# Kernel optimization log

Hardware: AMD Instinct MI355X
Metric: run time of the kernel (lower is better)

The kernel has to match this reference:

```python
import jax, jax.numpy as jnp
import numpy as np

NEG = -1000.0  # fill value for unmatched (type_mask != ti) entries

B, N, R = 4, 48, 16
T = 2 * R + 1          # 33 transition channels
Nc, L = 80, 3          # chains, chain length
Nt, Ni = 16, 5         # triples, chains per triple (uniform c_sections)


def setup_inputs() -> dict:
    key = jax.random.key(0)
    k1, k2, k3, k4, k5 = jax.random.split(key, 5)
    transitions = jax.random.normal(k1, (B, N, N, T), dtype=jnp.float32)
    type_mask = jax.random.randint(k2, (B, N, N, R), 0, 2, dtype=jnp.int32)
    rules = jax.random.randint(k3, (Nc, L), 0, T, dtype=jnp.int32)
    # stacked per-triple weights [Nt, Ni] (orig: ParameterList of [Ni,1]) and biases [Nt]
    weights = jax.random.normal(k4, (Nt, Ni), dtype=jnp.float32) / np.sqrt(Ni)
    biases = jax.random.uniform(k5, (Nt,), dtype=jnp.float32, minval=-1.0, maxval=1.0)
    return {"transitions": transitions, "type_mask": type_mask, "rules": rules,
            "weights": weights, "biases": biases}


def path_scores(transitions, rules):
    """Tropical (max-plus) chain DP.
    transitions: [B,N,N,T], rules: [Nc,L] -> scores [B,N,N,Nc]
    scores[b,x,y,c] = max over intermediate nodes of sum of hop scores.
    """
    Lc = rules.shape[1]
    hops = [transitions[..., rules[:, l]] for l in range(Lc)]  # each [B,N,N,Nc]
    # max-plus "matmul": s[b,x,y,c] = max_k hops0[b,x,k,c] + hops1[b,k,y,c]
    s = jnp.max(hops[0][:, :, :, None, :] + hops[1][:, None, :, :, :], axis=2)
    for l in range(2, Lc):
        s = jnp.max(s[:, :, :, None, :] + hops[l][:, None, :, :, :], axis=2)
    return s


def reference(transitions, type_mask, rules, weights, biases):
    # scores over all chains, exponentiated: [B,N,N,Nc]
    s = jnp.exp(path_scores(transitions, rules))
    # group chains by triple (uniform sections): [B,N,N,Nt,Ni]
    s = s.reshape(s.shape[0], s.shape[1], s.shape[2], Nt, Ni)
    # per-triple weighted sum + bias; one triple per relation so Nt == R
    comb = jnp.einsum('bxytc,tc->bxyt', s, weights) + biases  # [B,N,N,R]
    # masked_scatter: write score where type_mask[...,i] == ti (== 0 here), else -1000
    out = jnp.where(type_mask == 0, comb, NEG)
    return out
```

## Files before the change

### kernel.cpp

```cpp
#include <hip/hip_runtime.h>
#include <cmath>

#define BB 4
#define NN 48
#define PP (NN * NN)
#define NP 49
#define TT 33
#define RR 16
#define NC 80
#define NI 5
#define NEG (-1000.0f)

__global__ __launch_bounds__(256) void transpose_kernel(
    const float* __restrict__ trans,
    float*       __restrict__ tpose)
{
    __shared__ float tile[64 * TT];
    const int blk = blockIdx.x;
    const int b   = blk / 36;
    const int p0  = (blk - b * 36) * 64;

    const float4* src = (const float4*)(trans + ((size_t)b * PP + p0) * TT);
    for (int j = threadIdx.x; j < 64 * TT / 4; j += 256)
        ((float4*)tile)[j] = src[j];
    __syncthreads();

    for (int j = threadIdx.x; j < TT * 64; j += 256) {
        const int t  = j >> 6;
        const int pl = j & 63;
        tpose[((size_t)b * TT + t) * PP + p0 + pl] = tile[pl * TT + t];
    }
}

__global__ __launch_bounds__(192) void chain_dp_kernel(
    const float* __restrict__ tpose,
    const int*   __restrict__ rules,
    const float* __restrict__ weights,
    float*       __restrict__ sw)
{
    __shared__ float H0T[NN * NP];
    __shared__ float H1 [PP];
    __shared__ float H2 [PP];
    __shared__ float S1T[NN * NP];

    const int bc = blockIdx.x;
    const int b  = bc / NC;
    const int c  = bc - b * NC;

    const int r0 = rules[c * 3 + 0];
    const int r1 = rules[c * 3 + 1];
    const int r2 = rules[c * 3 + 2];

    const float* p0 = tpose + ((size_t)b * TT + r0) * PP;
    const float* p1 = tpose + ((size_t)b * TT + r1) * PP;
    const float* p2 = tpose + ((size_t)b * TT + r2) * PP;

    for (int j = threadIdx.x; j < PP / 4; j += 192) {
        ((float4*)H1)[j] = ((const float4*)p1)[j];
        ((float4*)H2)[j] = ((const float4*)p2)[j];
        const float4 v0 = ((const float4*)p0)[j];
        const int x = (4 * j) / NN;
        const int k = (4 * j) - x * NN;
        H0T[(k + 0) * NP + x] = v0.x;
        H0T[(k + 1) * NP + x] = v0.y;
        H0T[(k + 2) * NP + x] = v0.z;
        H0T[(k + 3) * NP + x] = v0.w;
    }
    __syncthreads();

    const int tx = threadIdx.x & 15;
    const int ty = threadIdx.x >> 4;
    const int x0 = tx * 3;
    const int y0 = ty * 4;

    float acc[3][4];
    #pragma unroll
    for (int jx = 0; jx < 3; ++jx)
        #pragma unroll
        for (int jy = 0; jy < 4; ++jy) acc[jx][jy] = -INFINITY;

    #pragma unroll 4
    for (int kp = 0; kp < NN / 2; ++kp) {
        const int k = kp * 2;
        float a0[3], a1[3];
        #pragma unroll
        for (int jx = 0; jx < 3; ++jx) {
            a0[jx] = H0T[k * NP + x0 + jx];
            a1[jx] = H0T[(k + 1) * NP + x0 + jx];
        }
        const float4 bv0 = *(const float4*)&H1[k * NN + y0];
        const float4 bv1 = *(const float4*)&H1[(k + 1) * NN + y0];
        const float b0[4] = {bv0.x, bv0.y, bv0.z, bv0.w};
        const float b1[4] = {bv1.x, bv1.y, bv1.z, bv1.w};
        #pragma unroll
        for (int jx = 0; jx < 3; ++jx)
            #pragma unroll
            for (int jy = 0; jy < 4; ++jy)
                acc[jx][jy] = fmaxf(acc[jx][jy],
                                    fmaxf(a0[jx] + b0[jy], a1[jx] + b1[jy]));
    }

    #pragma unroll
    for (int jx = 0; jx < 3; ++jx)
        #pragma unroll
        for (int jy = 0; jy < 4; ++jy)
            S1T[(y0 + jy) * NP + x0 + jx] = acc[jx][jy];
    __syncthreads();

    float acc2[3][4];
    #pragma unroll
    for (int jx = 0; jx < 3; ++jx)
        #pragma unroll
        for (int jy = 0; jy < 4; ++jy) acc2[jx][jy] = -INFINITY;

    #pragma unroll 4
    for (int kp = 0; kp < NN / 2; ++kp) {
        const int k = kp * 2;
        float a0[3], a1[3];
        #pragma unroll
        for (int jx = 0; jx < 3; ++jx) {
            a0[jx] = S1T[k * NP + x0 + jx];
            a1[jx] = S1T[(k + 1) * NP + x0 + jx];
        }
        const float4 bv0 = *(const float4*)&H2[k * NN + y0];
        const float4 bv1 = *(const float4*)&H2[(k + 1) * NN + y0];
        const float b0[4] = {bv0.x, bv0.y, bv0.z, bv0.w};
        const float b1[4] = {bv1.x, bv1.y, bv1.z, bv1.w};
        #pragma unroll
        for (int jx = 0; jx < 3; ++jx)
            #pragma unroll
            for (int jy = 0; jy < 4; ++jy)
                acc2[jx][jy] = fmaxf(acc2[jx][jy],
                                     fmaxf(a0[jx] + b0[jy], a1[jx] + b1[jy]));
    }

    const float wgt = weights[c];
    float* outp = sw + (size_t)bc * PP;
    #pragma unroll
    for (int jx = 0; jx < 3; ++jx) {
        float4 o;
        o.x = __expf(acc2[jx][0]) * wgt;
        o.y = __expf(acc2[jx][1]) * wgt;
        o.z = __expf(acc2[jx][2]) * wgt;
        o.w = __expf(acc2[jx][3]) * wgt;
        *(float4*)&outp[(x0 + jx) * NN + y0] = o;
    }
}

__global__ __launch_bounds__(256) void combine_kernel(
    const float* __restrict__ sw,
    const int*   __restrict__ mask,
    const float* __restrict__ biases,
    float*       __restrict__ out)
{
    const int tq = threadIdx.x >> 7;
    const int pl = blockIdx.x * 128 + (threadIdx.x & 127);
    if (pl >= BB * PP) return;
    const int b = pl / PP;
    const int p = pl - b * PP;

    const float* base = sw + (size_t)b * NC * PP + p;

    float acc[8];
    #pragma unroll
    for (int tt = 0; tt < 8; ++tt) {
        const int t = tq * 8 + tt;
        float s = biases[t];
        #pragma unroll
        for (int i = 0; i < NI; ++i)
            s += base[(size_t)(t * NI + i) * PP];
        acc[tt] = s;
    }

    const int4* m4 = (const int4*)(mask + (size_t)pl * RR + tq * 8);
    float4*     o4 = (float4*)(out + (size_t)pl * RR + tq * 8);
    #pragma unroll
    for (int q = 0; q < 2; ++q) {
        const int4 m = m4[q];
        float4 o;
        o.x = (m.x == 0) ? acc[q * 4 + 0] : NEG;
        o.y = (m.y == 0) ? acc[q * 4 + 1] : NEG;
        o.z = (m.z == 0) ? acc[q * 4 + 2] : NEG;
        o.w = (m.w == 0) ? acc[q * 4 + 3] : NEG;
        o4[q] = o;
    }
}

extern "C" void kernel_launch(void* const* d_in, const int* in_sizes, int n_in,
                              void* d_out, int out_size, void* d_ws, size_t ws_size,
                              hipStream_t stream)
{
    const float* trans   = (const float*)d_in[0];
    const int*   mask    = (const int*)  d_in[1];
    const int*   rules   = (const int*)  d_in[2];
    const float* weights = (const float*)d_in[3];
    const float* biases  = (const float*)d_in[4];
    float* out = (float*)d_out;

    float* tpose = (float*)d_ws;
    float* sw    = tpose + (size_t)BB * TT * PP;

    transpose_kernel<<<BB * 36, 256, 0, stream>>>(trans, tpose);

    chain_dp_kernel<<<BB * NC, 192, 0, stream>>>(tpose, rules, weights, sw);

    const int total2 = BB * PP * 2;
    combine_kernel<<<(total2 + 255) / 256, 256, 0, stream>>>(sw, mask, biases, out);
}
```

Measured before the change: 76.70 us.

## Split chain DP blocks by x-half and use row-major padded LDS tiles

Each (batch, chain) block is split into two blocks that each handle 24 rows of x, doubling the grid from 320 to 640 blocks so more CUs are busy. The left operand is now kept row-major with a padded stride, so float4 reads along k replace the transposed scalar stores, and each thread computes a 3x2 tile. The cost is that H1 and H2 are loaded twice, once per half-block, and register blocking per thread is smaller.

Measured after the change: 75.04 us (median of 2 runs). 1.02x faster.

```diff
diff --git a/kernel.cpp b/kernel.cpp
--- a/kernel.cpp
+++ b/kernel.cpp
@@ -4,13 +4,15 @@
 #define BB 4
 #define NN 48
 #define PP (NN * NN)
-#define NP 49
 #define TT 33
 #define RR 16
 #define NC 80
 #define NI 5
 #define NEG (-1000.0f)
 
+#define XH 24
+#define RS 52
+
 __global__ __launch_bounds__(256) void transpose_kernel(
     const float* __restrict__ trans,
     float*       __restrict__ tpose)
@@ -38,112 +40,119 @@
     const float* __restrict__ weights,
     float*       __restrict__ sw)
 {
-    __shared__ float H0T[NN * NP];
+    __shared__ float H0R[XH * RS];
     __shared__ float H1 [PP];
     __shared__ float H2 [PP];
-    __shared__ float S1T[NN * NP];
-
-    const int bc = blockIdx.x;
-    const int b  = bc / NC;
-    const int c  = bc - b * NC;
+    __shared__ float S1R[XH * RS];
+
+    const int blk = blockIdx.x;
+    const int bc  = blk >> 1;
+    const int xh  = blk & 1;
+    const int b   = bc / NC;
+    const int c   = bc - b * NC;
+    const int x0r = xh * XH;
 
     const int r0 = rules[c * 3 + 0];
     const int r1 = rules[c * 3 + 1];
     const int r2 = rules[c * 3 + 2];
 
-    const float* p0 = tpose + ((size_t)b * TT + r0) * PP;
+    const float* p0 = tpose + ((size_t)b * TT + r0) * PP + (size_t)x0r * NN;
     const float* p1 = tpose + ((size_t)b * TT + r1) * PP;
     const float* p2 = tpose + ((size_t)b * TT + r2) * PP;
 
     for (int j = threadIdx.x; j < PP / 4; j += 192) {
         ((float4*)H1)[j] = ((const float4*)p1)[j];
         ((float4*)H2)[j] = ((const float4*)p2)[j];
-        const float4 v0 = ((const float4*)p0)[j];
-        const int x = (4 * j) / NN;
-        const int k = (4 * j) - x * NN;
-        H0T[(k + 0) * NP + x] = v0.x;
-        H0T[(k + 1) * NP + x] = v0.y;
-        H0T[(k + 2) * NP + x] = v0.z;
-        H0T[(k + 3) * NP + x] = v0.w;
+    }
+    for (int j = threadIdx.x; j < XH * NN / 4; j += 192) {
+        const int row = j / 12;
+        const int cw  = j - row * 12;
+        *(float4*)&H0R[row * RS + cw * 4] = ((const float4*)p0)[j];
     }
     __syncthreads();
 
-    const int tx = threadIdx.x & 15;
-    const int ty = threadIdx.x >> 4;
-    const int x0 = tx * 3;
-    const int y0 = ty * 4;
-
-    float acc[3][4];
-    #pragma unroll
-    for (int jx = 0; jx < 3; ++jx)
-        #pragma unroll
-        for (int jy = 0; jy < 4; ++jy) acc[jx][jy] = -INFINITY;
+    const int yt = threadIdx.x % 24;
+    const int xt = threadIdx.x / 24;
+    const int x0 = xt * 3;
+    const int y0 = yt * 2;
+
+    float acc[3][2];
+    #pragma unroll
+    for (int jx = 0; jx < 3; ++jx) { acc[jx][0] = -INFINITY; acc[jx][1] = -INFINITY; }
 
     #pragma unroll 4
-    for (int kp = 0; kp < NN / 2; ++kp) {
-        const int k = kp * 2;
-        float a0[3], a1[3];
-        #pragma unroll
-        for (int jx = 0; jx < 3; ++jx) {
-            a0[jx] = H0T[k * NP + x0 + jx];
-            a1[jx] = H0T[(k + 1) * NP + x0 + jx];
-        }
-        const float4 bv0 = *(const float4*)&H1[k * NN + y0];
-        const float4 bv1 = *(const float4*)&H1[(k + 1) * NN + y0];
-        const float b0[4] = {bv0.x, bv0.y, bv0.z, bv0.w};
-        const float b1[4] = {bv1.x, bv1.y, bv1.z, bv1.w};
+    for (int k4 = 0; k4 < NN; k4 += 4) {
+        const float4 a0 = *(const float4*)&H0R[(x0 + 0) * RS + k4];
+        const float4 a1 = *(const float4*)&H0R[(x0 + 1) * RS + k4];
+        const float4 a2 = *(const float4*)&H0R[(x0 + 2) * RS + k4];
+        const float2 b0 = *(const float2*)&H1[(k4 + 0) * NN + y0];
+        const float2 b1 = *(const float2*)&H1[(k4 + 1) * NN + y0];
+        const float2 b2 = *(const float2*)&H1[(k4 + 2) * NN + y0];
+        const float2 b3 = *(const float2*)&H1[(k4 + 3) * NN + y0];
+        const float av[3][4] = {{a0.x, a0.y, a0.z, a0.w},
+                                {a1.x, a1.y, a1.z, a1.w},
+                                {a2.x, a2.y, a2.z, a2.w}};
+        const float bv[4][2] = {{b0.x, b0.y}, {b1.x, b1.y},
+                                {b2.x, b2.y}, {b3.x, b3.y}};
         #pragma unroll
         for (int jx = 0; jx < 3; ++jx)
             #pragma unroll
-            for (int jy = 0; jy < 4; ++jy)
-                acc[jx][jy] = fmaxf(acc[jx][jy],
-                                    fmaxf(a0[jx] + b0[jy], a1[jx] + b1[jy]));
-    }
-
-    #pragma unroll
-    for (int jx = 0; jx < 3; ++jx)
-        #pragma unroll
-        for (int jy = 0; jy < 4; ++jy)
-            S1T[(y0 + jy) * NP + x0 + jx] = acc[jx][jy];
+            for (int jy = 0; jy < 2; ++jy) {
+                const float s0 = av[jx][0] + bv[0][jy];
+                const float s1 = av[jx][1] + bv[1][jy];
+                const float s2 = av[jx][2] + bv[2][jy];
+                const float s3 = av[jx][3] + bv[3][jy];
+                acc[jx][jy] = fmaxf(acc[jx][jy], fmaxf(s0, s1));
+                acc[jx][jy] = fmaxf(acc[jx][jy], fmaxf(s2, s3));
+            }
+    }
+
+    #pragma unroll
+    for (int jx = 0; jx < 3; ++jx) {
+        float2 v; v.x = acc[jx][0]; v.y = acc[jx][1];
+        *(float2*)&S1R[(x0 + jx) * RS + y0] = v;
+    }
     __syncthreads();
 
-    float acc2[3][4];
-    #pragma unroll
-    for (int jx = 0; jx < 3; ++jx)
-        #pragma unroll
-        for (int jy = 0; jy < 4; ++jy) acc2[jx][jy] = -INFINITY;
+    float acc2[3][2];
+    #pragma unroll
+    for (int jx = 0; jx < 3; ++jx) { acc2[jx][0] = -INFINITY; acc2[jx][1] = -INFINITY; }
 
     #pragma unroll 4
-    for (int kp = 0; kp < NN / 2; ++kp) {
-        const int k = kp * 2;
-        float a0[3], a1[3];
-        #pragma unroll
-        for (int jx = 0; jx < 3; ++jx) {
-            a0[jx] = S1T[k * NP + x0 + jx];
-            a1[jx] = S1T[(k + 1) * NP + x0 + jx];
-        }
-        const float4 bv0 = *(const float4*)&H2[k * NN + y0];
-        const float4 bv1 = *(const float4*)&H2[(k + 1) * NN + y0];
-        const float b0[4] = {bv0.x, bv0.y, bv0.z, bv0.w};
-        const float b1[4] = {bv1.x, bv1.y, bv1.z, bv1.w};
+    for (int k4 = 0; k4 < NN; k4 += 4) {
+        const float4 a0 = *(const float4*)&S1R[(x0 + 0) * RS + k4];
+        const float4 a1 = *(const float4*)&S1R[(x0 + 1) * RS + k4];
+        const float4 a2 = *(const float4*)&S1R[(x0 + 2) * RS + k4];
+        const float2 b0 = *(const float2*)&H2[(k4 + 0) * NN + y0];
+        const float2 b1 = *(const float2*)&H2[(k4 + 1) * NN + y0];
+        const float2 b2 = *(const float2*)&H2[(k4 + 2) * NN + y0];
+        const float2 b3 = *(const float2*)&H2[(k4 + 3) * NN + y0];
+        const float av[3][4] = {{a0.x, a0.y, a0.z, a0.w},
+                                {a1.x, a1.y, a1.z, a1.w},
+                                {a2.x, a2.y, a2.z, a2.w}};
+        const float bv[4][2] = {{b0.x, b0.y}, {b1.x, b1.y},
+                                {b2.x, b2.y}, {b3.x, b3.y}};
         #pragma unroll
         for (int jx = 0; jx < 3; ++jx)
             #pragma unroll
-            for (int jy = 0; jy < 4; ++jy)
-                acc2[jx][jy] = fmaxf(acc2[jx][jy],
-                                     fmaxf(a0[jx] + b0[jy], a1[jx] + b1[jy]));
+            for (int jy = 0; jy < 2; ++jy) {
+                const float s0 = av[jx][0] + bv[0][jy];
+                const float s1 = av[jx][1] + bv[1][jy];
+                const float s2 = av[jx][2] + bv[2][jy];
+                const float s3 = av[jx][3] + bv[3][jy];
+                acc2[jx][jy] = fmaxf(acc2[jx][jy], fmaxf(s0, s1));
+                acc2[jx][jy] = fmaxf(acc2[jx][jy], fmaxf(s2, s3));
+            }
     }
 
     const float wgt = weights[c];
-    float* outp = sw + (size_t)bc * PP;
+    float* outp = sw + (size_t)bc * PP + (size_t)x0r * NN;
     #pragma unroll
     for (int jx = 0; jx < 3; ++jx) {
-        float4 o;
+        float2 o;
         o.x = __expf(acc2[jx][0]) * wgt;
         o.y = __expf(acc2[jx][1]) * wgt;
-        o.z = __expf(acc2[jx][2]) * wgt;
-        o.w = __expf(acc2[jx][3]) * wgt;
-        *(float4*)&outp[(x0 + jx) * NN + y0] = o;
+        *(float2*)&outp[(x0 + jx) * NN + y0] = o;
     }
 }
 
@@ -202,7 +211,7 @@
 
     transpose_kernel<<<BB * 36, 256, 0, stream>>>(trans, tpose);
 
-    chain_dp_kernel<<<BB * NC, 192, 0, stream>>>(tpose, rules, weights, sw);
+    chain_dp_kernel<<<BB * NC * 2, 192, 0, stream>>>(tpose, rules, weights, sw);
 
     const int total2 = BB * PP * 2;
     combine_kernel<<<(total2 + 255) / 256, 256, 0, stream>>>(sw, mask, biases, out);
```
